# Performance work log

Measured on AMD Instinct MI355X. Metric: run time of the kernel, lower is better.

The kernel has to match this reference:

```python
import jax, jax.numpy as jnp
import numpy as np

# ---------------- config (from ObjectDetector source) ----------------
B = 2; IMG = 224; STRIDE = 32; FH = IMG // STRIDE          # 7x7 feature map
C_FEAT = 1024
SIZES = (32., 64., 128., 256., 512.); RATIOS = (0.5, 1.0, 2.0)
A = len(SIZES) * len(RATIOS)                                # 15 anchors/loc
NA = FH * FH * A                                            # 735 anchors/img
PRE_NMS = min(1000, NA); POST_NMS = min(1000, NA)           # testing config
RPN_NMS_T = 0.7; RPN_MIN_SIZE = 1e-3
NUM_CLASSES = 37
ROI_OUT = 7; ROI_SR = 2; ROI_SCALE = 1.0 / STRIDE
REP = 1024
SCORE_T = 0.05; DET_NMS_T = 0.5; DETS_PER_IMG = 100
CAND_K = 2048            # candidate cap before final batched NMS
MIN_SIZE_DET = 1e-2
BBOX_CLIP = float(np.log(1000.0 / 16.0))


def make_anchors():
    scales = np.array(SIZES, np.float32); ratios = np.array(RATIOS, np.float32)
    h_r = np.sqrt(ratios); w_r = 1.0 / h_r
    ws = (w_r[:, None] * scales[None, :]).reshape(-1)
    hs = (h_r[:, None] * scales[None, :]).reshape(-1)
    base = np.round(np.stack([-ws, -hs, ws, hs], 1) / 2.0)   # [A,4]
    sy, sx = np.meshgrid(np.arange(FH) * STRIDE, np.arange(FH) * STRIDE, indexing='ij')
    shifts = np.stack([sx.reshape(-1), sy.reshape(-1), sx.reshape(-1), sy.reshape(-1)], 1).astype(np.float32)
    return jnp.asarray((shifts[:, None, :] + base[None, :, :]).reshape(-1, 4))  # [NA,4] (H,W,A)


def conv(x, w, b, stride=1, pad=0):
    y = jax.lax.conv_general_dilated(x, w, (stride, stride), [(pad, pad)] * 2,
                                     dimension_numbers=('NCHW', 'OIHW', 'NCHW'))
    return y + b[None, :, None, None]


def decode_boxes(deltas, boxes, weights):
    wx, wy, ww, wh = weights
    w = boxes[..., 2] - boxes[..., 0]; h = boxes[..., 3] - boxes[..., 1]
    cx = boxes[..., 0] + 0.5 * w; cy = boxes[..., 1] + 0.5 * h
    dx = deltas[..., 0] / wx; dy = deltas[..., 1] / wy
    dw = jnp.minimum(deltas[..., 2] / ww, BBOX_CLIP)
    dh = jnp.minimum(deltas[..., 3] / wh, BBOX_CLIP)
    pcx = dx * w + cx; pcy = dy * h + cy
    pw = jnp.exp(dw) * w; ph = jnp.exp(dh) * h
    return jnp.stack([pcx - 0.5 * pw, pcy - 0.5 * ph, pcx + 0.5 * pw, pcy + 0.5 * ph], -1)


def clip_boxes(b):
    x = jnp.clip(b[..., 0::2], 0.0, float(IMG)); y = jnp.clip(b[..., 1::2], 0.0, float(IMG))
    return jnp.stack([x[..., 0], y[..., 0], x[..., 1], y[..., 1]], -1)


def box_iou(a, b):
    area_a = (a[:, 2] - a[:, 0]) * (a[:, 3] - a[:, 1])
    area_b = (b[:, 2] - b[:, 0]) * (b[:, 3] - b[:, 1])
    lt = jnp.maximum(a[:, None, :2], b[None, :, :2])
    rb = jnp.minimum(a[:, None, 2:], b[None, :, 2:])
    wh = jnp.clip(rb - lt, 0.0, None)
    inter = wh[..., 0] * wh[..., 1]
    return inter / jnp.maximum(area_a[:, None] + area_b[None, :] - inter, 1e-9)


def nms_keep(boxes, scores, thresh):
    """Greedy NMS; returns keep mask in original order (fixed shapes)."""
    n = boxes.shape[0]
    order = jnp.argsort(-scores)
    iou = box_iou(*(jax.lax.stop_gradient(boxes[order]),) * 2)
    idx = jnp.arange(n)
    def body(i, keep):
        sup = (iou[i] > thresh) & (idx > i) & keep[i]
        return keep & ~sup
    keep_sorted = jax.lax.fori_loop(0, n, body, jnp.ones(n, bool))
    return jnp.zeros(n, bool).at[order].set(keep_sorted)


def rpn_filter_one(obj_logits, deltas, anchors):
    # obj_logits [NA], deltas [NA,4] (detached, as in torchvision RPN)
    top_v, top_i = jax.lax.top_k(obj_logits, PRE_NMS)
    boxes = clip_boxes(decode_boxes(deltas[top_i], anchors[top_i], (1., 1., 1., 1.)))
    prob = jax.nn.sigmoid(top_v)
    ws = boxes[:, 2] - boxes[:, 0]; hs = boxes[:, 3] - boxes[:, 1]
    prob = jnp.where((ws >= RPN_MIN_SIZE) & (hs >= RPN_MIN_SIZE), prob, -1.0)
    prob = jnp.where(nms_keep(boxes, prob, RPN_NMS_T), prob, -1.0)
    sv, si = jax.lax.top_k(prob, POST_NMS)
    return boxes[si], sv > 0.0


def bilinear(f_hwc, ys, xs):
    # torchvision roi_align bilinear sampling; f_hwc [H,W,C], ys/xs [R,O]
    H, W, _ = f_hwc.shape
    vy = (ys >= -1.0) & (ys <= H); vx = (xs >= -1.0) & (xs <= W)
    y = jnp.clip(ys, 0.0, None); x = jnp.clip(xs, 0.0, None)
    y0 = jnp.minimum(jnp.floor(y).astype(jnp.int32), H - 1)
    x0 = jnp.minimum(jnp.floor(x).astype(jnp.int32), W - 1)
    y1 = jnp.minimum(y0 + 1, H - 1); x1 = jnp.minimum(x0 + 1, W - 1)
    y = jnp.where(y0 == H - 1, y0.astype(y.dtype), y)
    x = jnp.where(x0 == W - 1, x0.astype(x.dtype), x)
    ly = y - y0; lx = x - x0; hy = 1.0 - ly; hx = 1.0 - lx
    g = lambda yi, xi: f_hwc[yi[:, :, None], xi[:, None, :]]   # [R,O,O,C]
    val = ((hy[:, :, None] * hx[:, None, :])[..., None] * g(y0, x0)
         + (hy[:, :, None] * lx[:, None, :])[..., None] * g(y0, x1)
         + (ly[:, :, None] * hx[:, None, :])[..., None] * g(y1, x0)
         + (ly[:, :, None] * lx[:, None, :])[..., None] * g(y1, x1))
    return val * (vy[:, :, None] & vx[:, None, :])[..., None]


def roi_align_one(feat_chw, rois):
    # feat [C,H,W], rois [R,4] -> [R,C,7,7]; output_size=7, sampling_ratio=2, scale=1/32
    f = jnp.transpose(feat_chw, (1, 2, 0))
    x1 = rois[:, 0] * ROI_SCALE; y1 = rois[:, 1] * ROI_SCALE
    rw = jnp.maximum(rois[:, 2] * ROI_SCALE - x1, 1.0)
    rh = jnp.maximum(rois[:, 3] * ROI_SCALE - y1, 1.0)
    bw = rw / ROI_OUT; bh = rh / ROI_OUT
    grid = jnp.arange(ROI_OUT, dtype=jnp.float32)
    acc = 0.0
    for iy in range(ROI_SR):
        ys = y1[:, None] + (grid[None, :] + (iy + 0.5) / ROI_SR) * bh[:, None]
        for ix in range(ROI_SR):
            xs = x1[:, None] + (grid[None, :] + (ix + 0.5) / ROI_SR) * bw[:, None]
            acc = acc + bilinear(f, ys, xs)
    return jnp.transpose(acc / (ROI_SR * ROI_SR), (0, 3, 1, 2))


def postprocess_one(logits, box_deltas, proposals, roi_valid):
    R = logits.shape[0]
    scores = jax.nn.softmax(logits, -1)
    boxes = clip_boxes(decode_boxes(box_deltas.reshape(R, NUM_CLASSES, 4),
                                    proposals[:, None, :], (10., 10., 5., 5.)))
    boxes = boxes[:, 1:, :].reshape(-1, 4)       # drop background class
    scores = jnp.where(roi_valid[:, None], scores[:, 1:], 0.0).reshape(-1)
    labels = jnp.broadcast_to(jnp.arange(1, NUM_CLASSES)[None, :], (R, NUM_CLASSES - 1)).reshape(-1)
    ws = boxes[:, 2] - boxes[:, 0]; hs = boxes[:, 3] - boxes[:, 1]
    ok = (ws >= MIN_SIZE_DET) & (hs >= MIN_SIZE_DET) & (scores > SCORE_T)
    cs, ci = jax.lax.top_k(jnp.where(ok, scores, -1.0), CAND_K)
    cb = boxes[ci]; cl = labels[ci]
    off = cl.astype(cb.dtype) * (IMG + 1.0)      # batched (per-class) NMS trick
    keep = nms_keep(cb + off[:, None], cs, DET_NMS_T)
    tv, ti = jax.lax.top_k(jnp.where(keep, cs, -1.0), DETS_PER_IMG)
    valid = tv > 0.0
    out_boxes = jnp.where(valid[:, None], cb[ti], 0.0)
    out_scores = jnp.where(valid, tv, 0.0)
    out_labels = jnp.where(valid, cl[ti], 0).astype(out_boxes.dtype)
    return jnp.concatenate([out_boxes, out_scores[:, None], out_labels[:, None]], -1)  # [100,6]


def forward(images, params, anchors):
    (bb_w, bb_b, rpn_w, rpn_b, cls_w, cls_b, reg_w, reg_b,
     fc1_w, fc1_b, fc2_w, fc2_b, clsp_w, clsp_b, boxp_w, boxp_b) = params
    Bn = images.shape[0]
    feats = jax.nn.relu(conv(images, bb_w, bb_b, stride=STRIDE))        # [B,1024,7,7]
    t = jax.nn.relu(conv(feats, rpn_w, rpn_b, stride=1, pad=1))
    obj = jnp.transpose(conv(t, cls_w, cls_b), (0, 2, 3, 1)).reshape(Bn, -1)            # [B,NA]
    reg = jnp.transpose(conv(t, reg_w, reg_b).reshape(Bn, A, 4, FH, FH),
                        (0, 3, 4, 1, 2)).reshape(Bn, -1, 4)                              # [B,NA,4]
    obj_d = jax.lax.stop_gradient(obj); reg_d = jax.lax.stop_gradient(reg)  # RPN detaches
    proposals, roi_valid = jax.vmap(lambda o, d: rpn_filter_one(o, d, anchors))(obj_d, reg_d)
    pooled = jax.vmap(roi_align_one)(feats, proposals)                  # [B,R,1024,7,7]
    x = pooled.reshape(Bn * POST_NMS, -1)
    x = jax.nn.relu(x @ fc1_w.T + fc1_b)
    x = jax.nn.relu(x @ fc2_w.T + fc2_b)
    logits = (x @ clsp_w.T + clsp_b).reshape(Bn, POST_NMS, NUM_CLASSES)
    bdelt = (x @ boxp_w.T + boxp_b).reshape(Bn, POST_NMS, NUM_CLASSES * 4)
    return jax.vmap(postprocess_one)(logits, bdelt, proposals, roi_valid)  # [B,100,6]


def setup_inputs() -> dict:
    key = jax.random.key(0)
    ks = jax.random.split(key, 10)
    w = lambda k, shape, s=0.02: jax.random.normal(k, shape, jnp.float32) * s
    return {
        'images': jax.random.uniform(ks[0], (B, 1, IMG, IMG), jnp.float32),
        'bb_w': w(ks[1], (C_FEAT, 1, STRIDE, STRIDE)), 'bb_b': jnp.zeros((C_FEAT,), jnp.float32),
        'rpn_w': w(ks[2], (C_FEAT, C_FEAT, 3, 3)), 'rpn_b': jnp.zeros((C_FEAT,), jnp.float32),
        'cls_w': w(ks[3], (A, C_FEAT, 1, 1)), 'cls_b': jnp.zeros((A,), jnp.float32),
        'reg_w': w(ks[4], (4 * A, C_FEAT, 1, 1)), 'reg_b': jnp.zeros((4 * A,), jnp.float32),
        'fc1_w': w(ks[5], (REP, C_FEAT * ROI_OUT * ROI_OUT), 0.005), 'fc1_b': jnp.zeros((REP,), jnp.float32),
        'fc2_w': w(ks[6], (REP, REP)), 'fc2_b': jnp.zeros((REP,), jnp.float32),
        'clsp_w': w(ks[7], (NUM_CLASSES, REP)), 'clsp_b': jnp.zeros((NUM_CLASSES,), jnp.float32),
        'boxp_w': w(ks[8], (NUM_CLASSES * 4, REP)), 'boxp_b': jnp.zeros((NUM_CLASSES * 4,), jnp.float32),
    }


def reference(images, bb_w, bb_b, rpn_w, rpn_b, cls_w, cls_b, reg_w, reg_b,
              fc1_w, fc1_b, fc2_w, fc2_b, clsp_w, clsp_b, boxp_w, boxp_b):
    anchors = make_anchors()
    params = (bb_w, bb_b, rpn_w, rpn_b, cls_w, cls_b, reg_w, reg_b,
              fc1_w, fc1_b, fc2_w, fc2_b, clsp_w, clsp_b, boxp_w, boxp_b)
    return forward(images, params, anchors)
```

## Files before the change

### kernel.cpp

```cpp
#include <hip/hip_runtime.h>
#include <math.h>

#define NANCH 735
#define NCAND 26460
#define NCANDP 26624
#define BBCLIP 4.135166556742356f
#define KF1 4864
#define KHALF 2432

typedef short bf16x8 __attribute__((ext_vector_type(8)));
typedef float f32x4 __attribute__((ext_vector_type(4)));

__device__ __forceinline__ unsigned short f2b(float f) {
  unsigned int u = __float_as_uint(f);
  unsigned int r = (u >> 16) & 1u;
  u += 0x7fffu + r;
  return (unsigned short)(u >> 16);
}

__device__ __forceinline__ bool before_(float va, int ia, float vb, int ib) {
  return (va > vb) || (va == vb && ia < ib);
}

template<int NTOT, int NTH>
__device__ void bitonic_sort_sh(float* v, int* id) {
  const int t = threadIdx.x;
  for (int k = 2; k <= NTOT; k <<= 1) {
    for (int j = k >> 1; j > 0; j >>= 1) {
      for (int s = t; s < NTOT; s += NTH) {
        int p = s ^ j;
        if (p > s) {
          float v1 = v[s], v2 = v[p];
          int i1 = id[s], i2 = id[p];
          bool up = ((s & k) == 0);
          if (before_(v2, i2, v1, i1) == up) {
            v[s] = v2; id[s] = i2; v[p] = v1; id[p] = i1;
          }
        }
      }
      __syncthreads();
    }
  }
}

template<int NTOT, int NTH>
__device__ void bitonic_merge_sh(float* v, int* id) {
  const int t = threadIdx.x;
  for (int j = NTOT >> 1; j > 0; j >>= 1) {
    for (int s = t; s < NTOT; s += NTH) {
      int p = s ^ j;
      if (p > s) {
        float v1 = v[s], v2 = v[p];
        int i1 = id[s], i2 = id[p];
        if (before_(v2, i2, v1, i1)) {
          v[s] = v2; id[s] = i2; v[p] = v1; id[p] = i1;
        }
      }
    }
    __syncthreads();
  }
}

__global__ void k_anchors(float* __restrict__ anchors) {
  int i = blockIdx.x * 64 + threadIdx.x;
  if (i >= NANCH) return;
  int pos = i / 15, a = i % 15;
  int iy = pos / 7, ix = pos % 7;
  int rr = a / 5, sc = a % 5;
  double ratio = (rr == 0) ? 0.5 : (rr == 1 ? 1.0 : 2.0);
  double scale = (double)(32 << sc);
  double hr = sqrt(ratio), wr = 1.0 / hr;
  double wsz = wr * scale, hsz = hr * scale;
  float bx1 = (float)rint(-wsz * 0.5), by1 = (float)rint(-hsz * 0.5);
  float bx2 = (float)rint(wsz * 0.5),  by2 = (float)rint(hsz * 0.5);
  float sx = (float)(ix * 32), sy = (float)(iy * 32);
  float* o = anchors + (size_t)i * 4;
  o[0] = sx + bx1; o[1] = sy + by1; o[2] = sx + bx2; o[3] = sy + by2;
}

__global__ void k_im2col_bb(const float* __restrict__ images, float* __restrict__ patch) {
  int i = blockIdx.x * 256 + threadIdx.x;
  if (i >= 98 * 1024) return;
  int rowi = i >> 10, k = i & 1023;
  int b = rowi / 49, pos = rowi % 49;
  int oy = pos / 7, ox = pos % 7;
  int ky = k >> 5, kx = k & 31;
  patch[i] = images[((size_t)b * 224 + oy * 32 + ky) * 224 + ox * 32 + kx];
}

__global__ void k_transpose_feats(const float* __restrict__ bbC, float* __restrict__ ft) {
  int i = blockIdx.x * 256 + threadIdx.x;
  if (i >= 2 * 1024 * 49) return;
  int b = i / (1024 * 49);
  int rem = i % (1024 * 49);
  int c = rem / 49, q = rem % 49;
  ft[i] = bbC[((size_t)b * 49 + q) * 1024 + c];
}

__global__ void k_im2col_rpn(const float* __restrict__ ft, float* __restrict__ im2) {
  int i = blockIdx.x * 256 + threadIdx.x;
  if (i >= 98 * 9216) return;
  int rowi = i / 9216, k = i % 9216;
  int b = rowi / 49, pos = rowi % 49;
  int oy = pos / 7, ox = pos % 7;
  int ic = k / 9, kk = k % 9;
  int ky = kk / 3, kx = kk % 3;
  int y = oy + ky - 1, x = ox + kx - 1;
  float v = 0.f;
  if ((unsigned)y < 7u && (unsigned)x < 7u)
    v = ft[((size_t)b * 1024 + ic) * 49 + y * 7 + x];
  im2[i] = v;
}

__global__ __launch_bounds__(256) void k_gemm32(
    const float* __restrict__ A, int lda, int M,
    const float* __restrict__ B, int ldb,
    float* __restrict__ P, int N, int Kchunk)
{
  __shared__ float As[2][16][68];
  __shared__ float Bs[2][16][68];
  const int m0 = blockIdx.x * 64, n0 = blockIdx.y * 64;
  const int t = threadIdx.x;
  const long long k0 = (long long)blockIdx.z * Kchunk;
  float acc[4][4];
#pragma unroll
  for (int i = 0; i < 4; ++i)
#pragma unroll
    for (int j = 0; j < 4; ++j) acc[i][j] = 0.f;
  const int tm = (t >> 4) * 4;
  const int tn = (t & 15) * 4;
  const int sm = t >> 4, sk = t & 15;
  const int gmA = m0 + sm;
  auto ldA = [&](int mo, long long kk) -> float {
    int gm = gmA + mo;
    return (gm < M) ? A[(size_t)gm * lda + k0 + kk + sk] : 0.f;
  };
  auto ldB = [&](int mo, long long kk) -> float {
    return B[(size_t)(n0 + sm + mo) * ldb + k0 + kk + sk];
  };
  const int nt = Kchunk >> 4;
  float a0 = ldA(0, 0), a1 = ldA(16, 0), a2 = ldA(32, 0), a3 = ldA(48, 0);
  float b0 = ldB(0, 0), b1 = ldB(16, 0), b2 = ldB(32, 0), b3 = ldB(48, 0);
  int cur = 0;
  for (int it = 0; it < nt; ++it) {
    As[cur][sk][sm] = a0; As[cur][sk][sm + 16] = a1;
    As[cur][sk][sm + 32] = a2; As[cur][sk][sm + 48] = a3;
    Bs[cur][sk][sm] = b0; Bs[cur][sk][sm + 16] = b1;
    Bs[cur][sk][sm + 32] = b2; Bs[cur][sk][sm + 48] = b3;
    __syncthreads();
    if (it + 1 < nt) {
      long long kk = (long long)(it + 1) * 16;
      a0 = ldA(0, kk); a1 = ldA(16, kk); a2 = ldA(32, kk); a3 = ldA(48, kk);
      b0 = ldB(0, kk); b1 = ldB(16, kk); b2 = ldB(32, kk); b3 = ldB(48, kk);
    }
#pragma unroll
    for (int k = 0; k < 16; ++k) {
      float av[4], bv[4];
#pragma unroll
      for (int i = 0; i < 4; ++i) av[i] = As[cur][k][tm + i];
#pragma unroll
      for (int j = 0; j < 4; ++j) bv[j] = Bs[cur][k][tn + j];
#pragma unroll
      for (int i = 0; i < 4; ++i)
#pragma unroll
        for (int j = 0; j < 4; ++j) acc[i][j] = fmaf(av[i], bv[j], acc[i][j]);
    }
    cur ^= 1;
  }
  float* Pp = P + (size_t)blockIdx.z * M * N;
#pragma unroll
  for (int i = 0; i < 4; ++i) {
    int gm = m0 + tm + i;
    if (gm < M) {
#pragma unroll
      for (int j = 0; j < 4; ++j)
        Pp[(size_t)gm * N + n0 + tn + j] = acc[i][j];
    }
  }
}

__global__ __launch_bounds__(256) void k_gemm_bf16(
    const unsigned short* __restrict__ A, int lda, int M,
    const unsigned short* __restrict__ B, int ldb,
    float* __restrict__ P, int N, int Kchunk,
    const int* __restrict__ nvalid)
{
  __shared__ __attribute__((aligned(16))) unsigned short As[2][128][40];
  __shared__ __attribute__((aligned(16))) unsigned short Bs[2][128][40];
  const int G = gridDim.x * gridDim.y * gridDim.z;
  int lid = blockIdx.x + gridDim.x * (blockIdx.y + gridDim.y * blockIdx.z);
  lid = (lid & 7) * (G >> 3) + (lid >> 3);
  const int bx = lid % gridDim.x;
  const int rest = lid / gridDim.x;
  const int by = rest % gridDim.y, bz = rest / gridDim.y;
  const int m0 = bx * 128, n0 = by * 128;
  if (nvalid) {
    int nv0 = nvalid[0], nv1 = nvalid[1];
    bool ok = (m0 < nv0) || ((m0 + 128 > NANCH) && (m0 < NANCH + nv1));
    if (!ok) return;
  }
  const int t = threadIdx.x;
  const int lane = t & 63, wid = t >> 6;
  const int wm = (wid >> 1) * 64, wn = (wid & 1) * 64;
  const size_t k0 = (size_t)bz * Kchunk;
  f32x4 acc[4][4];
#pragma unroll
  for (int i = 0; i < 4; ++i)
#pragma unroll
    for (int j = 0; j < 4; ++j) acc[i][j] = (f32x4){0.f, 0.f, 0.f, 0.f};
  const int r0 = t >> 2, c0 = (t & 3) * 8;
  const int fr = lane & 15, fk = (lane >> 4) * 8;
  const int gmA0 = m0 + r0, gmA1 = m0 + r0 + 64;
  const bool vA0 = gmA0 < M, vA1 = gmA1 < M;
  const unsigned short* pA0 = A + (size_t)gmA0 * lda + k0 + c0;
  const unsigned short* pA1 = A + (size_t)gmA1 * lda + k0 + c0;
  const unsigned short* pB0 = B + (size_t)(n0 + r0) * ldb + k0 + c0;
  const unsigned short* pB1 = B + (size_t)(n0 + r0 + 64) * ldb + k0 + c0;
  bf16x8 rA0 = {}, rA1 = {}, rB0, rB1;
  if (vA0) rA0 = *(const bf16x8*)pA0;
  if (vA1) rA1 = *(const bf16x8*)pA1;
  rB0 = *(const bf16x8*)pB0;
  rB1 = *(const bf16x8*)pB1;
  const int nt = Kchunk >> 5;
  int cur = 0;
  for (int it = 0; it < nt; ++it) {
    *(bf16x8*)&As[cur][r0][c0] = rA0;
    *(bf16x8*)&As[cur][r0 + 64][c0] = rA1;
    *(bf16x8*)&Bs[cur][r0][c0] = rB0;
    *(bf16x8*)&Bs[cur][r0 + 64][c0] = rB1;
    __syncthreads();
    if (it + 1 < nt) {
      size_t ofs = (size_t)(it + 1) * 32;
      rA0 = vA0 ? *(const bf16x8*)(pA0 + ofs) : (bf16x8){};
      rA1 = vA1 ? *(const bf16x8*)(pA1 + ofs) : (bf16x8){};
      rB0 = *(const bf16x8*)(pB0 + ofs);
      rB1 = *(const bf16x8*)(pB1 + ofs);
    }
    bf16x8 af[4], bg[4];
#pragma unroll
    for (int i = 0; i < 4; ++i) af[i] = *(const bf16x8*)&As[cur][wm + i * 16 + fr][fk];
#pragma unroll
    for (int j = 0; j < 4; ++j) bg[j] = *(const bf16x8*)&Bs[cur][wn + j * 16 + fr][fk];
#pragma unroll
    for (int i = 0; i < 4; ++i)
#pragma unroll
      for (int j = 0; j < 4; ++j)
        acc[i][j] = __builtin_amdgcn_mfma_f32_16x16x32_bf16(af[i], bg[j], acc[i][j], 0, 0, 0);
    cur ^= 1;
  }
  float* Pp = P + (size_t)bz * M * N;
#pragma unroll
  for (int i = 0; i < 4; ++i) {
#pragma unroll
    for (int r = 0; r < 4; ++r) {
      int gm = m0 + wm + i * 16 + (lane >> 4) * 4 + r;
      if (gm < M) {
#pragma unroll
        for (int j = 0; j < 4; ++j)
          Pp[(size_t)gm * N + n0 + wn + j * 16 + (lane & 15)] = acc[i][j][r];
      }
    }
  }
}

__global__ __launch_bounds__(256) void k_gemm_mb(
    const unsigned short* __restrict__ A,
    const unsigned short* __restrict__ W1p,
    float* __restrict__ Mb)
{
  __shared__ __attribute__((aligned(16))) unsigned short As[2][128][40];
  __shared__ __attribute__((aligned(16))) unsigned short Bs[2][128][40];
  const int G = gridDim.x * gridDim.y * gridDim.z;
  int lid = blockIdx.x + gridDim.x * (blockIdx.y + gridDim.y * blockIdx.z);
  lid = (lid & 7) * (G >> 3) + (lid >> 3);
  const int rest = lid;
  const int by = rest % gridDim.y, p = rest / gridDim.y;
  const int n0 = by * 128;
  const int M = 98;
  const unsigned short* B = W1p + (size_t)p * 1048576;
  const int t = threadIdx.x;
  const int lane = t & 63, wid = t >> 6;
  const int wm = (wid >> 1) * 64, wn = (wid & 1) * 64;
  f32x4 acc[4][4];
#pragma unroll
  for (int i = 0; i < 4; ++i)
#pragma unroll
    for (int j = 0; j < 4; ++j) acc[i][j] = (f32x4){0.f, 0.f, 0.f, 0.f};
  const int r0 = t >> 2, c0 = (t & 3) * 8;
  const int fr = lane & 15, fk = (lane >> 4) * 8;
  int gA0 = r0; if (gA0 >= M) gA0 = M - 1;
  int gA1 = r0 + 64; if (gA1 >= M) gA1 = M - 1;
  const unsigned short* pA0 = A + (size_t)gA0 * 1024 + c0;
  const unsigned short* pA1 = A + (size_t)gA1 * 1024 + c0;
  const unsigned short* pB0 = B + (size_t)(n0 + r0) * 1024 + c0;
  const unsigned short* pB1 = B + (size_t)(n0 + r0 + 64) * 1024 + c0;
  bf16x8 rA0 = *(const bf16x8*)pA0;
  bf16x8 rA1 = *(const bf16x8*)pA1;
  bf16x8 rB0 = *(const bf16x8*)pB0;
  bf16x8 rB1 = *(const bf16x8*)pB1;
  const int nt = 1024 >> 5;
  int cur = 0;
  for (int it = 0; it < nt; ++it) {
    *(bf16x8*)&As[cur][r0][c0] = rA0;
    *(bf16x8*)&As[cur][r0 + 64][c0] = rA1;
    *(bf16x8*)&Bs[cur][r0][c0] = rB0;
    *(bf16x8*)&Bs[cur][r0 + 64][c0] = rB1;
    __syncthreads();
    if (it + 1 < nt) {
      size_t ofs = (size_t)(it + 1) * 32;
      rA0 = *(const bf16x8*)(pA0 + ofs);
      rA1 = *(const bf16x8*)(pA1 + ofs);
      rB0 = *(const bf16x8*)(pB0 + ofs);
      rB1 = *(const bf16x8*)(pB1 + ofs);
    }
    bf16x8 af[4], bg[4];
#pragma unroll
    for (int i = 0; i < 4; ++i) af[i] = *(const bf16x8*)&As[cur][wm + i * 16 + fr][fk];
#pragma unroll
    for (int j = 0; j < 4; ++j) bg[j] = *(const bf16x8*)&Bs[cur][wn + j * 16 + fr][fk];
#pragma unroll
    for (int i = 0; i < 4; ++i)
#pragma unroll
      for (int j = 0; j < 4; ++j)
        acc[i][j] = __builtin_amdgcn_mfma_f32_16x16x32_bf16(af[i], bg[j], acc[i][j], 0, 0, 0);
    cur ^= 1;
  }
  float* Pp = Mb + (size_t)p * 98 * 1024;
#pragma unroll
  for (int i = 0; i < 4; ++i) {
#pragma unroll
    for (int r = 0; r < 4; ++r) {
      int gm = wm + i * 16 + (lane >> 4) * 4 + r;
      if (gm < M) {
#pragma unroll
        for (int j = 0; j < 4; ++j)
          Pp[(size_t)gm * 1024 + n0 + wn + j * 16 + (lane & 15)] = acc[i][j][r];
      }
    }
  }
}

__global__ __launch_bounds__(256) void k_mtrans(const float* __restrict__ Mb,
                                                unsigned short* __restrict__ Bmat)
{
  __shared__ float tile[98][129];
  const int p = blockIdx.x, n0 = blockIdx.y * 128;
  const int t = threadIdx.x;
  for (int j = t; j < 98 * 128; j += 256) {
    int q = j >> 7, nl = j & 127;
    tile[q][nl] = Mb[((size_t)p * 98 + q) * 1024 + n0 + nl];
  }
  __syncthreads();
  for (int j = t; j < 128 * 98; j += 256) {
    int nl = j / 98, q2 = j % 98;
    int bb = q2 >= 49 ? 1 : 0;
    int col = bb * KHALF + p * 49 + (q2 - bb * 49);
    Bmat[(size_t)(n0 + nl) * KF1 + col] = f2b(tile[q2][nl]);
  }
  if (p == 0) {
    for (int j = t; j < 128 * 62; j += 256) {
      int nl = j / 62, e = j % 62;
      int bb = e >= 31 ? 1 : 0;
      int col = bb * KHALF + 2401 + (e - bb * 31);
      Bmat[(size_t)(n0 + nl) * KF1 + col] = 0;
    }
  }
}

__global__ __launch_bounds__(256) void k_gbuild(const float* __restrict__ props,
                                                unsigned short* __restrict__ Gmat)
{
#pragma clang fp contract(off)
  int rg = blockIdx.x;
  int b = rg / NANCH;
  __shared__ float g[KF1];
  int t = threadIdx.x;
  for (int j = t; j < KF1; j += 256) g[j] = 0.f;
  __syncthreads();
  if (t < 49) {
    const float* roi = props + (size_t)rg * 4;
    int p = t, oy = p / 7, ox = p % 7;
    float x1 = roi[0] * 0.03125f, y1 = roi[1] * 0.03125f;
    float rw = fmaxf(roi[2] * 0.03125f - x1, 1.f);
    float rh = fmaxf(roi[3] * 0.03125f - y1, 1.f);
    float bw = rw / 7.f, bh = rh / 7.f;
    float* gb = g + b * KHALF + p * 49;
    for (int iy = 0; iy < 2; ++iy) {
      for (int ix = 0; ix < 2; ++ix) {
        float ys = y1 + ((float)oy + ((float)iy + 0.5f) * 0.5f) * bh;
        float xs = x1 + ((float)ox + ((float)ix + 0.5f) * 0.5f) * bw;
        bool vy = (ys >= -1.f) && (ys <= 7.f);
        bool vx = (xs >= -1.f) && (xs <= 7.f);
        float yc = fmaxf(ys, 0.f), xc = fmaxf(xs, 0.f);
        int y0 = min((int)floorf(yc), 6), x0 = min((int)floorf(xc), 6);
        int y1i = min(y0 + 1, 6), x1i = min(x0 + 1, 6);
        if (y0 == 6) yc = 6.f;
        if (x0 == 6) xc = 6.f;
        float ly = yc - (float)y0, lx = xc - (float)x0;
        float hy = 1.f - ly, hx = 1.f - lx;
        float vm = (vy && vx) ? 0.25f : 0.f;
        gb[y0 * 7 + x0]   += hy * hx * vm;
        gb[y0 * 7 + x1i]  += hy * lx * vm;
        gb[y1i * 7 + x0]  += ly * hx * vm;
        gb[y1i * 7 + x1i] += ly * lx * vm;
      }
    }
  }
  __syncthreads();
  unsigned short* Gr = Gmat + (size_t)rg * KF1;
  for (int j = t; j < KF1; j += 256) Gr[j] = f2b(g[j]);
}

__global__ void k_reduce(const float* __restrict__ P, float* __restrict__ dst,
                         unsigned short* __restrict__ dst16,
                         int S, int M, int N, const float* __restrict__ bias, int flags)
{
  size_t i = (size_t)blockIdx.x * 256 + threadIdx.x;
  size_t tot = (size_t)M * N;
  if (i >= tot) return;
  float v = (flags & 1) ? 0.f : dst[i];
  for (int s = 0; s < S; ++s) v += P[(size_t)s * tot + i];
  if (flags & 2) v += bias[i % (size_t)N];
  if (flags & 4) v = fmaxf(v, 0.f);
  dst[i] = v;
  if (flags & 8) dst16[i] = f2b(v);
}

__global__ void k_f2b(const float* __restrict__ s, unsigned short* __restrict__ d, int n) {
  int i = (blockIdx.x * 256 + threadIdx.x) * 4;
  if (i >= n) return;
  float4 v = *(const float4*)(s + i);
  ushort4 o;
  o.x = f2b(v.x); o.y = f2b(v.y); o.z = f2b(v.z); o.w = f2b(v.w);
  *(ushort4*)(d + i) = o;
}

__global__ __launch_bounds__(256) void k_w1perm2(const float* __restrict__ w,
                                                 unsigned short* __restrict__ o)
{
  __shared__ unsigned short tile[128 * 50];
  const int n = blockIdx.x, ct = blockIdx.y;
  const float* src = w + (size_t)n * 50176 + (size_t)ct * 128 * 49;
  const int t = threadIdx.x;
  for (int i = t; i < 6272; i += 256) {
    int cl = i / 49, p = i % 49;
    tile[cl * 50 + p] = f2b(src[i]);
  }
  __syncthreads();
  for (int j = t; j < 6272; j += 256) {
    int p = j >> 7, cl = j & 127;
    o[((size_t)p * 1024 + n) * 1024 + (size_t)ct * 128 + cl] = tile[cl * 50 + p];
  }
}

__global__ __launch_bounds__(256) void k_rpn_head(
    const float* __restrict__ tmn, const float* __restrict__ cls_w,
    const float* __restrict__ cls_b, const float* __restrict__ reg_w,
    const float* __restrict__ reg_b, float* __restrict__ obj, float* __restrict__ reg)
{
  int blk = blockIdx.x;
  __shared__ float col[1024];
  const float* row = tmn + (size_t)blk * 1024;
  for (int i = threadIdx.x; i < 1024; i += 256) col[i] = row[i];
  __syncthreads();
  int b = blk / 49, pos = blk % 49;
  for (int o = threadIdx.x; o < 75; o += 256) {
    const float* w = (o < 15) ? (cls_w + (size_t)o * 1024) : (reg_w + (size_t)(o - 15) * 1024);
    float s = 0.f;
    for (int k = 0; k < 1024; ++k) s = fmaf(col[k], w[k], s);
    if (o < 15) {
      obj[(size_t)b * NANCH + pos * 15 + o] = s + cls_b[o];
    } else {
      int c = o - 15, a = c >> 2, d = c & 3;
      reg[((size_t)b * NANCH + pos * 15 + a) * 4 + d] = s + reg_b[c];
    }
  }
}

__global__ __launch_bounds__(1024) void k_rpn_prep(
    const float* __restrict__ obj, const float* __restrict__ reg,
    const float* __restrict__ anchors,
    float* __restrict__ bxp, float* __restrict__ pnms)
{
#pragma clang fp contract(off)
  const int b = blockIdx.x, t = threadIdx.x;
  __shared__ float sval[1024];
  __shared__ float vo1[1024];
  __shared__ int o1a[1024];
  __shared__ int wtv[16];
  __shared__ int wti[16];
  sval[t] = (t < NANCH) ? obj[(size_t)b * NANCH + t] : -INFINITY;
  __syncthreads();
  {
    float v = sval[t];
    int rank = 0;
    for (int j = 0; j < NANCH; ++j) {
      float u = sval[j];
      rank += (u > v) || (u == v && j < t);
    }
    if (t < NANCH) { vo1[rank] = v; o1a[rank] = t; }
  }
  __syncthreads();
  float x1 = 0.f, y1 = 0.f, x2 = 0.f, y2 = 0.f, prob = -1.f;
  bool flag = false;
  if (t < NANCH) {
    int ai = o1a[t];
    const float* d = reg + ((size_t)b * NANCH + ai) * 4;
    const float* an = anchors + (size_t)ai * 4;
    float aw = an[2] - an[0], ah = an[3] - an[1];
    float acx = an[0] + 0.5f * aw, acy = an[1] + 0.5f * ah;
    float dw = fminf(d[2], BBCLIP), dh = fminf(d[3], BBCLIP);
    float pcx = d[0] * aw + acx, pcy = d[1] * ah + acy;
    float pw = expf(dw) * aw, ph = expf(dh) * ah;
    x1 = pcx - 0.5f * pw; y1 = pcy - 0.5f * ph;
    x2 = pcx + 0.5f * pw; y2 = pcy + 0.5f * ph;
    x1 = fminf(fmaxf(x1, 0.f), 224.f);
    y1 = fminf(fmaxf(y1, 0.f), 224.f);
    x2 = fminf(fmaxf(x2, 0.f), 224.f);
    y2 = fminf(fmaxf(y2, 0.f), 224.f);
    flag = (x2 - x1 >= 1e-3f) && (y2 - y1 >= 1e-3f);
    prob = 1.f / (1.f + expf(-vo1[t]));
  }
  bool iflag = (t < NANCH) && !flag;
  unsigned long long balv = __ballot(flag);
  unsigned long long bali = __ballot(iflag);
  int lane = t & 63, w = t >> 6;
  if (lane == 0) { wtv[w] = __popcll(balv); wti[w] = __popcll(bali); }
  __syncthreads();
  int nval = 0, basev = 0, basei = 0;
  for (int k = 0; k < 16; ++k) {
    int cv = wtv[k], ci = wti[k];
    nval += cv;
    if (k < w) { basev += cv; basei += ci; }
  }
  if (t < NANCH) {
    unsigned long long lm = (1ull << lane) - 1;
    int pos = flag ? (basev + __popcll(balv & lm))
                   : (nval + basei + __popcll(bali & lm));
    float* o = bxp + ((size_t)b * NANCH + pos) * 4;
    o[0] = x1; o[1] = y1; o[2] = x2; o[3] = y2;
    pnms[(size_t)b * NANCH + pos] = flag ? prob : -1.f;
  }
}

__global__ __launch_bounds__(256) void k_rpn_mask(
    const float* __restrict__ bxp, unsigned long long* __restrict__ rmask)
{
#pragma clang fp contract(off)
  int blk = blockIdx.x;
  int b = blk / 35;
  int row = (blk % 35) * 21 + (int)(threadIdx.x / 12);
  int w = threadIdx.x % 12;
  if (threadIdx.x >= 252 || row >= NANCH) return;
  const float* a = bxp + ((size_t)b * NANCH + row) * 4;
  float a0 = a[0], a1 = a[1], a2 = a[2], a3 = a[3];
  float aarea = (a2 - a0) * (a3 - a1);
  int l0 = w * 64;
  int l1 = (l0 + 64 < NANCH) ? l0 + 64 : NANCH;
  int ls = (l0 > row + 1) ? l0 : row + 1;
  unsigned long long bits = 0ull;
  for (int l = ls; l < l1; ++l) {
    const float* q = bxp + ((size_t)b * NANCH + l) * 4;
    float b0 = q[0], b1 = q[1], b2 = q[2], b3 = q[3];
    float barea = (b2 - b0) * (b3 - b1);
    float ix1 = fmaxf(a0, b0), iy1 = fmaxf(a1, b1);
    float ix2 = fminf(a2, b2), iy2 = fminf(a3, b3);
    float iw = fmaxf(ix2 - ix1, 0.f), ih = fmaxf(iy2 - iy1, 0.f);
    float inter = iw * ih;
    float iou = inter / fmaxf(aarea + barea - inter, 1e-9f);
    if (iou > 0.7f) bits |= 1ull << (l & 63);
  }
  rmask[((size_t)b * NANCH + row) * 12 + w] = bits;
}

__global__ __launch_bounds__(1024) void k_rpn_fin(
    const float* __restrict__ bxp, const float* __restrict__ pnms,
    const unsigned long long* __restrict__ rmask,
    float* __restrict__ props, int* __restrict__ meta)
{
  const int b = blockIdx.x, t = threadIdx.x;
  __shared__ unsigned long long smask[NANCH * 12];
  __shared__ float sp[1024];
  __shared__ unsigned long long keepw[12];
  __shared__ int wtot[16];
  for (int i = t; i < NANCH * 12; i += 1024)
    smask[i] = rmask[(size_t)b * NANCH * 12 + i];
  sp[t] = (t < NANCH) ? pnms[(size_t)b * NANCH + t] : -1.f;
  __syncthreads();
  if (t < 64) {
    unsigned long long kl = (t < 12) ? ~0ull : 0ull;
    for (int i = 0; i < NANCH; ++i) {
      unsigned long long kw = __shfl(kl, i >> 6);
      unsigned long long m = (t < 12) ? smask[i * 12 + t] : 0ull;
      bool on = (kw >> (i & 63)) & 1ull;
      kl &= on ? ~m : ~0ull;
    }
    if (t < 12) keepw[t] = kl;
  }
  __syncthreads();
  bool flag = false;
  if (t < NANCH) {
    bool kp = (keepw[t >> 6] >> (t & 63)) & 1ull;
    flag = kp && (sp[t] > 0.f);
  }
  unsigned long long bal = __ballot(flag);
  int lane = t & 63, w = t >> 6;
  if (lane == 0) wtot[w] = __popcll(bal);
  __syncthreads();
  int base = 0, tot = 0;
  for (int k = 0; k < 16; ++k) { int c = wtot[k]; if (k < w) base += c; tot += c; }
  if (flag) {
    int pos = base + __popcll(bal & ((1ull << lane) - 1));
    const float* src = bxp + ((size_t)b * NANCH + t) * 4;
    float* o = props + ((size_t)b * NANCH + pos) * 4;
    o[0] = src[0]; o[1] = src[1]; o[2] = src[2]; o[3] = src[3];
  }
  if (t == 0) meta[b] = tot;
}

__global__ __launch_bounds__(256) void k_heads(
    const float* __restrict__ h2, const float* __restrict__ cw,
    const float* __restrict__ cb, const float* __restrict__ bw_,
    const float* __restrict__ bb_, const int* __restrict__ meta,
    float* __restrict__ logits, float* __restrict__ bdelt)
{
  int rg = blockIdx.x;
  int b = rg / NANCH, r = rg % NANCH;
  if (r >= meta[b]) return;
  __shared__ float row[1024];
  for (int i = threadIdx.x; i < 1024; i += 256) row[i] = h2[(size_t)rg * 1024 + i];
  __syncthreads();
  for (int o = threadIdx.x; o < 185; o += 256) {
    const float* w = (o < 37) ? (cw + (size_t)o * 1024) : (bw_ + (size_t)(o - 37) * 1024);
    float s = 0.f;
    for (int k = 0; k < 1024; ++k) s = fmaf(row[k], w[k], s);
    if (o < 37) logits[(size_t)rg * 37 + o] = s + cb[o];
    else bdelt[(size_t)rg * 148 + (o - 37)] = s + bb_[o - 37];
  }
}

__global__ void k_cand(const float* __restrict__ logits, const float* __restrict__ bdelt,
                       const float* __restrict__ props, const int* __restrict__ meta,
                       float* __restrict__ cscore, float* __restrict__ cbox)
{
#pragma clang fp contract(off)
  int rg = blockIdx.x * blockDim.x + threadIdx.x;
  if (rg >= 2 * NANCH) return;
  int b = rg / NANCH, r = rg % NANCH;
  float* cs = cscore + (size_t)b * NCANDP;
  float* cb = cbox + (size_t)b * NCANDP * 4;
  int base = r * 36;
  if (r >= meta[b]) {
    for (int j = 0; j < 36; ++j) {
      cs[base + j] = -1.f;
      float* q = cb + (size_t)(base + j) * 4;
      q[0] = 0.f; q[1] = 0.f; q[2] = 0.f; q[3] = 0.f;
    }
    return;
  }
  const float* lg = logits + (size_t)rg * 37;
  float mx = lg[0];
// ... 86 lines not shown
      bitonic_merge_sh<2048, 1024>(Lv, Li);
    }
  }
  for (int s = t; s < 2048; s += 1024) {
    sel_score[b * 2048 + s] = Lv[s];
    sel_cidx[b * 2048 + s] = Li[s];
  }
  if (t == 0) meta[2 + b] = 2048;
}

__global__ void k_detmask(const int* __restrict__ sel_cidx,
                          const float* __restrict__ cbox,
                          const int* __restrict__ meta,
                          unsigned long long* __restrict__ dmask)
{
#pragma clang fp contract(off)
  int blk = blockIdx.x;
  int b = blk >> 8, row0 = (blk & 255) * 8;
  int npos = meta[2 + b];
  if (row0 >= npos) return;
  int t = threadIdx.x;
  int i = row0 + (t >> 5), w = t & 31;
  if (i >= npos) return;
  int ci = sel_cidx[b * 2048 + i];
  const float* bp = cbox + ((size_t)b * NCANDP + ci) * 4;
  float off = (float)(ci % 36 + 1) * 225.f;
  float a0 = bp[0] + off, a1 = bp[1] + off, a2 = bp[2] + off, a3 = bp[3] + off;
  float aarea = (a2 - a0) * (a3 - a1);
  unsigned long long bits = 0ull;
  int l0 = w * 64;
  int l1 = (l0 + 64 < npos) ? l0 + 64 : npos;
  int ls = (l0 > i + 1) ? l0 : i + 1;
  for (int l = ls; l < l1; ++l) {
    int cl = sel_cidx[b * 2048 + l];
    const float* q = cbox + ((size_t)b * NCANDP + cl) * 4;
    float o2 = (float)(cl % 36 + 1) * 225.f;
    float b0 = q[0] + o2, b1 = q[1] + o2, b2 = q[2] + o2, b3 = q[3] + o2;
    float barea = (b2 - b0) * (b3 - b1);
    float ix1 = fmaxf(a0, b0), iy1 = fmaxf(a1, b1);
    float ix2 = fminf(a2, b2), iy2 = fminf(a3, b3);
    float iw = fmaxf(ix2 - ix1, 0.f), ih = fmaxf(iy2 - iy1, 0.f);
    float inter = iw * ih;
    float iou = inter / fmaxf(aarea + barea - inter, 1e-9f);
    if (iou > 0.5f) bits |= 1ull << (l & 63);
  }
  dmask[((size_t)b * 2048 + i) * 32 + w] = bits;
}

__global__ __launch_bounds__(1024) void k_final(
    const float* __restrict__ sel_score, const int* __restrict__ sel_cidx,
    const float* __restrict__ cbox, const unsigned long long* __restrict__ dmask,
    const int* __restrict__ meta, float* __restrict__ out)
{
  const int b = blockIdx.x, t = threadIdx.x;
  __shared__ unsigned long long keepw[32];
  __shared__ float sv[2048];
  __shared__ float kv[2048]; __shared__ int ks[2048];
  __shared__ int wtot[32];
  int npos = meta[2 + b];
  for (int h = 0; h < 2; ++h) {
    int s = h * 1024 + t;
    sv[s] = sel_score[b * 2048 + s];
  }
  __syncthreads();
  if (t < 64) {
    unsigned long long kl = (t < 32) ? ~0ull : 0ull;
    for (int i = 0; i < npos; ++i) {
      unsigned long long kw = __shfl(kl, i >> 6);
      unsigned long long m = (t < 32) ? dmask[((size_t)b * 2048 + i) * 32 + t] : 0ull;
      bool on = (kw >> (i & 63)) & 1ull;
      kl &= on ? ~m : ~0ull;
    }
    if (t < 32) keepw[t] = kl;
  }
  __syncthreads();
  const int lane = t & 63, w = t >> 6;
  int s0 = t;
  bool f0 = ((keepw[s0 >> 6] >> (s0 & 63)) & 1ull) && (sv[s0] > 0.f);
  unsigned long long bal0 = __ballot(f0);
  if (lane == 0) wtot[w] = __popcll(bal0);
  int s1 = 1024 + t;
  bool f1 = ((keepw[s1 >> 6] >> (s1 & 63)) & 1ull) && (sv[s1] > 0.f);
  unsigned long long bal1 = __ballot(f1);
  if (lane == 0) wtot[16 + w] = __popcll(bal1);
  __syncthreads();
  int nk = 0, base0 = 0, base1 = 0;
  for (int k = 0; k < 32; ++k) {
    int c = wtot[k];
    if (k < w) base0 += c;
    if (k < 16 + w) base1 += c;
    nk += c;
  }
  int p0 = -1, p1 = -1;
  if (f0) { p0 = base0 + __popcll(bal0 & ((1ull << lane) - 1)); kv[p0] = sv[s0]; ks[p0] = s0; }
  if (f1) { p1 = base1 + __popcll(bal1 & ((1ull << lane) - 1)); kv[p1] = sv[s1]; ks[p1] = s1; }
  __syncthreads();
  if (f0) {
    float v = sv[s0]; int rank = 0;
    for (int j = 0; j < nk; ++j) { float u = kv[j]; int ju = ks[j]; rank += (u > v) || (u == v && ju < s0); }
    if (rank < 100) {
      int ci = sel_cidx[b * 2048 + s0];
      const float* bp = cbox + ((size_t)b * NCANDP + ci) * 4;
      float* o = out + ((size_t)b * 100 + rank) * 6;
      o[0] = bp[0]; o[1] = bp[1]; o[2] = bp[2]; o[3] = bp[3];
      o[4] = v; o[5] = (float)(ci % 36 + 1);
    }
  }
  if (f1) {
    float v = sv[s1]; int rank = 0;
    for (int j = 0; j < nk; ++j) { float u = kv[j]; int ju = ks[j]; rank += (u > v) || (u == v && ju < s1); }
    if (rank < 100) {
      int ci = sel_cidx[b * 2048 + s1];
      const float* bp = cbox + ((size_t)b * NCANDP + ci) * 4;
      float* o = out + ((size_t)b * 100 + rank) * 6;
      o[0] = bp[0]; o[1] = bp[1]; o[2] = bp[2]; o[3] = bp[3];
      o[4] = v; o[5] = (float)(ci % 36 + 1);
    }
  }
  if (t < 100 && t >= nk) {
    float* o = out + ((size_t)b * 100 + t) * 6;
    o[0] = 0.f; o[1] = 0.f; o[2] = 0.f; o[3] = 0.f; o[4] = 0.f; o[5] = 0.f;
  }
}

extern "C" void kernel_launch(void* const* d_in, const int* in_sizes, int n_in,
                              void* d_out, int out_size, void* d_ws, size_t ws_size,
                              hipStream_t stream)
{
  (void)in_sizes; (void)n_in; (void)out_size; (void)ws_size;
  const float* images = (const float*)d_in[0];
  const float* bb_w   = (const float*)d_in[1];
  const float* bb_b   = (const float*)d_in[2];
  const float* rpn_w  = (const float*)d_in[3];
  const float* rpn_b  = (const float*)d_in[4];
  const float* cls_w  = (const float*)d_in[5];
  const float* cls_b  = (const float*)d_in[6];
  const float* reg_w  = (const float*)d_in[7];
  const float* reg_b  = (const float*)d_in[8];
  const float* fc1_w  = (const float*)d_in[9];
  const float* fc1_b  = (const float*)d_in[10];
  const float* fc2_w  = (const float*)d_in[11];
  const float* fc2_b  = (const float*)d_in[12];
  const float* clsp_w = (const float*)d_in[13];
  const float* clsp_b = (const float*)d_in[14];
  const float* boxp_w = (const float*)d_in[15];
  const float* boxp_b = (const float*)d_in[16];
  float* out = (float*)d_out;
  char* ws = (char*)d_ws;

  size_t off = 0;
  auto alloc = [&](size_t bytes) -> size_t {
    size_t o = off; off = (off + bytes + 255) & ~(size_t)255; return o;
  };
  size_t o_anch  = alloc(735ull * 4 * 4);
  size_t o_patch = alloc(98ull * 1024 * 4);
  size_t o_bbC   = alloc(98ull * 1024 * 4);
  size_t o_bbh   = alloc(98ull * 1024 * 2);
  size_t o_ft    = alloc(2ull * 1024 * 49 * 4);
  size_t o_t     = alloc(98ull * 1024 * 4);
  size_t o_im2   = alloc(98ull * 9216 * 4);
  size_t o_obj   = alloc(1470ull * 4);
  size_t o_reg   = alloc(1470ull * 16);
  size_t o_props = alloc(1470ull * 16);
  size_t o_bxp   = alloc(1470ull * 16);
  size_t o_pnms  = alloc(1470ull * 4);
  size_t o_rm    = alloc(1470ull * 12 * 8);
  size_t o_meta  = alloc(256);
  size_t o_y1    = alloc(1470ull * 1024 * 4);
  size_t o_y2    = alloc(1470ull * 1024 * 4);
  size_t o_log   = alloc(1470ull * 37 * 4);
  size_t o_bd    = alloc(1470ull * 148 * 4);
  size_t o_cs    = alloc(2ull * NCANDP * 4);
  size_t o_cb    = alloc(2ull * NCANDP * 16);
  size_t o_ss    = alloc(2ull * 2048 * 4);
  size_t o_sc    = alloc(2ull * 2048 * 4);
  size_t o_dm    = alloc(2ull * 2048 * 32 * 8);
  size_t o_w1p   = alloc(51380224ull * 2);
  size_t o_mbuf  = alloc(49ull * 98 * 1024 * 4);
  size_t o_bmat  = alloc(1024ull * KF1 * 2);
  size_t o_gmat  = alloc(1470ull * KF1 * 2);
  size_t o_w2b   = alloc(1048576ull * 2);
  size_t o_y1b   = alloc(1470ull * 1024 * 2);
  size_t o_P     = alloc(32ull * 98 * 1024 * 4 > 4ull * 1470 * 1024 * 4
                         ? 32ull * 98 * 1024 * 4 : 4ull * 1470 * 1024 * 4);

  float* anch  = (float*)(ws + o_anch);
  float* patch = (float*)(ws + o_patch);
  float* bbC   = (float*)(ws + o_bbC);
  unsigned short* bbh = (unsigned short*)(ws + o_bbh);
  float* ft    = (float*)(ws + o_ft);
  float* tb    = (float*)(ws + o_t);
  float* im2   = (float*)(ws + o_im2);
  float* objb  = (float*)(ws + o_obj);
  float* regb  = (float*)(ws + o_reg);
  float* props = (float*)(ws + o_props);
  float* bxp   = (float*)(ws + o_bxp);
  float* pnms  = (float*)(ws + o_pnms);
  unsigned long long* rmb = (unsigned long long*)(ws + o_rm);
  int*   meta  = (int*)(ws + o_meta);
  float* y1    = (float*)(ws + o_y1);
  float* y2    = (float*)(ws + o_y2);
  float* logb  = (float*)(ws + o_log);
  float* bdb   = (float*)(ws + o_bd);
  float* csb   = (float*)(ws + o_cs);
  float* cbb   = (float*)(ws + o_cb);
  float* ssb   = (float*)(ws + o_ss);
  int*   scb   = (int*)(ws + o_sc);
  unsigned long long* dmb = (unsigned long long*)(ws + o_dm);
  unsigned short* w1p = (unsigned short*)(ws + o_w1p);
  float* mbuf  = (float*)(ws + o_mbuf);
  unsigned short* bmat = (unsigned short*)(ws + o_bmat);
  unsigned short* gmat = (unsigned short*)(ws + o_gmat);
  unsigned short* w2b = (unsigned short*)(ws + o_w2b);
  unsigned short* y1b = (unsigned short*)(ws + o_y1b);
  float* Pb    = (float*)(ws + o_P);

  k_anchors<<<12, 64, 0, stream>>>(anch);
  k_w1perm2<<<dim3(1024, 8), 256, 0, stream>>>(fc1_w, w1p);
  k_f2b<<<1024, 256, 0, stream>>>(fc2_w, w2b, 1048576);
  k_im2col_bb<<<392, 256, 0, stream>>>(images, patch);
  k_gemm32<<<dim3(2, 16, 16), 256, 0, stream>>>(patch, 1024, 98, bb_w, 1024, Pb, 1024, 64);
  k_reduce<<<392, 256, 0, stream>>>(Pb, bbC, bbh, 16, 98, 1024, bb_b, 15);
  k_transpose_feats<<<392, 256, 0, stream>>>(bbC, ft);
  k_gemm_mb<<<dim3(1, 8, 49), 256, 0, stream>>>(bbh, w1p, mbuf);
  k_mtrans<<<dim3(49, 8), 256, 0, stream>>>(mbuf, bmat);
  k_im2col_rpn<<<3528, 256, 0, stream>>>(ft, im2);
  k_gemm32<<<dim3(2, 16, 32), 256, 0, stream>>>(im2, 9216, 98, rpn_w, 9216, Pb, 1024, 288);
  k_reduce<<<392, 256, 0, stream>>>(Pb, tb, nullptr, 32, 98, 1024, rpn_b, 7);
  k_rpn_head<<<98, 256, 0, stream>>>(tb, cls_w, cls_b, reg_w, reg_b, objb, regb);
  k_rpn_prep<<<2, 1024, 0, stream>>>(objb, regb, anch, bxp, pnms);
  k_rpn_mask<<<70, 256, 0, stream>>>(bxp, rmb);
  k_rpn_fin<<<2, 1024, 0, stream>>>(bxp, pnms, rmb, props, meta);
  k_gbuild<<<1470, 256, 0, stream>>>(props, gmat);
  k_gemm_bf16<<<dim3(12, 8, 4), 256, 0, stream>>>(gmat, KF1, 1470, bmat, KF1, Pb, 1024, 1216, meta);
  k_reduce<<<5880, 256, 0, stream>>>(Pb, y1, y1b, 4, 1470, 1024, fc1_b, 15);
  k_gemm_bf16<<<dim3(12, 8, 2), 256, 0, stream>>>(y1b, 1024, 1470, w2b, 1024, Pb, 1024, 512, meta);
  k_reduce<<<5880, 256, 0, stream>>>(Pb, y2, nullptr, 2, 1470, 1024, fc2_b, 7);
  k_heads<<<1470, 256, 0, stream>>>(y2, clsp_w, clsp_b, boxp_w, boxp_b, meta, logb, bdb);
  k_cand<<<6, 256, 0, stream>>>(logb, bdb, props, meta, csb, cbb);
  k_top2048<<<2, 1024, 0, stream>>>(csb, ssb, scb, meta);
  k_detmask<<<512, 256, 0, stream>>>(scb, cbb, meta, dmb);
  k_final<<<2, 1024, 0, stream>>>(ssb, scb, cbb, dmb, meta, out);
}
```

Baseline: 523.0 us.

## Move backbone and RPN conv GEMMs to bf16 MFMA and drop transposes

Replaces the fp32 SIMT GEMM for the backbone patch conv and the 3x3 RPN conv with the existing bf16 MFMA GEMM, converting both weight tensors to bf16 on every call. The im2col buffers become bf16 and the RPN im2col reads the bf16 backbone features directly, which removes the feature transpose kernel. Anchors are now computed inline in the RPN prep kernel, so the anchor kernel and its buffer are gone. In exchange, each call pays for converting about 10M rpn weights, and conv precision drops to bf16, which could shift proposal scores and therefore NMS results.

```diff
diff --git a/kernel.cpp b/kernel.cpp
--- a/kernel.cpp
+++ b/kernel.cpp
@@ -16,6 +16,20 @@
   unsigned int r = (u >> 16) & 1u;
   u += 0x7fffu + r;
   return (unsigned short)(u >> 16);
+}
+
+__device__ __forceinline__ void anchor_of(int i, float* o) {
+  int pos = i / 15, a = i % 15;
+  int iy = pos / 7, ix = pos % 7;
+  int rr = a / 5, sc = a % 5;
+  double ratio = (rr == 0) ? 0.5 : (rr == 1 ? 1.0 : 2.0);
+  double scale = (double)(32 << sc);
+  double hr = sqrt(ratio), wr = 1.0 / hr;
+  double wsz = wr * scale, hsz = hr * scale;
+  float bx1 = (float)rint(-wsz * 0.5), by1 = (float)rint(-hsz * 0.5);
+  float bx2 = (float)rint(wsz * 0.5),  by2 = (float)rint(hsz * 0.5);
+  float sx = (float)(ix * 32), sy = (float)(iy * 32);
+  o[0] = sx + bx1; o[1] = sy + by1; o[2] = sx + bx2; o[3] = sy + by2;
 }
 
 __device__ __forceinline__ bool before_(float va, int ia, float vb, int ib) {
@@ -61,43 +75,18 @@
   }
 }
 
-__global__ void k_anchors(float* __restrict__ anchors) {
-  int i = blockIdx.x * 64 + threadIdx.x;
-  if (i >= NANCH) return;
-  int pos = i / 15, a = i % 15;
-  int iy = pos / 7, ix = pos % 7;
-  int rr = a / 5, sc = a % 5;
-  double ratio = (rr == 0) ? 0.5 : (rr == 1 ? 1.0 : 2.0);
-  double scale = (double)(32 << sc);
-  double hr = sqrt(ratio), wr = 1.0 / hr;
-  double wsz = wr * scale, hsz = hr * scale;
-  float bx1 = (float)rint(-wsz * 0.5), by1 = (float)rint(-hsz * 0.5);
-  float bx2 = (float)rint(wsz * 0.5),  by2 = (float)rint(hsz * 0.5);
-  float sx = (float)(ix * 32), sy = (float)(iy * 32);
-  float* o = anchors + (size_t)i * 4;
-  o[0] = sx + bx1; o[1] = sy + by1; o[2] = sx + bx2; o[3] = sy + by2;
-}
-
-__global__ void k_im2col_bb(const float* __restrict__ images, float* __restrict__ patch) {
+__global__ void k_im2col_bb(const float* __restrict__ images, unsigned short* __restrict__ patch) {
   int i = blockIdx.x * 256 + threadIdx.x;
   if (i >= 98 * 1024) return;
   int rowi = i >> 10, k = i & 1023;
   int b = rowi / 49, pos = rowi % 49;
   int oy = pos / 7, ox = pos % 7;
   int ky = k >> 5, kx = k & 31;
-  patch[i] = images[((size_t)b * 224 + oy * 32 + ky) * 224 + ox * 32 + kx];
-}
-
-__global__ void k_transpose_feats(const float* __restrict__ bbC, float* __restrict__ ft) {
-  int i = blockIdx.x * 256 + threadIdx.x;
-  if (i >= 2 * 1024 * 49) return;
-  int b = i / (1024 * 49);
-  int rem = i % (1024 * 49);
-  int c = rem / 49, q = rem % 49;
-  ft[i] = bbC[((size_t)b * 49 + q) * 1024 + c];
-}
-
-__global__ void k_im2col_rpn(const float* __restrict__ ft, float* __restrict__ im2) {
+  patch[i] = f2b(images[((size_t)b * 224 + oy * 32 + ky) * 224 + ox * 32 + kx]);
+}
+
+__global__ void k_im2col_rpn(const unsigned short* __restrict__ bbh,
+                             unsigned short* __restrict__ im2) {
   int i = blockIdx.x * 256 + threadIdx.x;
   if (i >= 98 * 9216) return;
   int rowi = i / 9216, k = i % 9216;
@@ -106,77 +95,10 @@
   int ic = k / 9, kk = k % 9;
   int ky = kk / 3, kx = kk % 3;
   int y = oy + ky - 1, x = ox + kx - 1;
-  float v = 0.f;
+  unsigned short v = 0;
   if ((unsigned)y < 7u && (unsigned)x < 7u)
-    v = ft[((size_t)b * 1024 + ic) * 49 + y * 7 + x];
+    v = bbh[((size_t)(b * 49 + y * 7 + x)) * 1024 + ic];
   im2[i] = v;
-}
-
-__global__ __launch_bounds__(256) void k_gemm32(
-    const float* __restrict__ A, int lda, int M,
-    const float* __restrict__ B, int ldb,
-    float* __restrict__ P, int N, int Kchunk)
-{
-  __shared__ float As[2][16][68];
-  __shared__ float Bs[2][16][68];
-  const int m0 = blockIdx.x * 64, n0 = blockIdx.y * 64;
-  const int t = threadIdx.x;
-  const long long k0 = (long long)blockIdx.z * Kchunk;
-  float acc[4][4];
-#pragma unroll
-  for (int i = 0; i < 4; ++i)
-#pragma unroll
-    for (int j = 0; j < 4; ++j) acc[i][j] = 0.f;
-  const int tm = (t >> 4) * 4;
-  const int tn = (t & 15) * 4;
-  const int sm = t >> 4, sk = t & 15;
-  const int gmA = m0 + sm;
-  auto ldA = [&](int mo, long long kk) -> float {
-    int gm = gmA + mo;
-    return (gm < M) ? A[(size_t)gm * lda + k0 + kk + sk] : 0.f;
-  };
-  auto ldB = [&](int mo, long long kk) -> float {
-    return B[(size_t)(n0 + sm + mo) * ldb + k0 + kk + sk];
-  };
-  const int nt = Kchunk >> 4;
-  float a0 = ldA(0, 0), a1 = ldA(16, 0), a2 = ldA(32, 0), a3 = ldA(48, 0);
-  float b0 = ldB(0, 0), b1 = ldB(16, 0), b2 = ldB(32, 0), b3 = ldB(48, 0);
-  int cur = 0;
-  for (int it = 0; it < nt; ++it) {
-    As[cur][sk][sm] = a0; As[cur][sk][sm + 16] = a1;
-    As[cur][sk][sm + 32] = a2; As[cur][sk][sm + 48] = a3;
-    Bs[cur][sk][sm] = b0; Bs[cur][sk][sm + 16] = b1;
-    Bs[cur][sk][sm + 32] = b2; Bs[cur][sk][sm + 48] = b3;
-    __syncthreads();
-    if (it + 1 < nt) {
-      long long kk = (long long)(it + 1) * 16;
-      a0 = ldA(0, kk); a1 = ldA(16, kk); a2 = ldA(32, kk); a3 = ldA(48, kk);
-      b0 = ldB(0, kk); b1 = ldB(16, kk); b2 = ldB(32, kk); b3 = ldB(48, kk);
-    }
-#pragma unroll
-    for (int k = 0; k < 16; ++k) {
-      float av[4], bv[4];
-#pragma unroll
-      for (int i = 0; i < 4; ++i) av[i] = As[cur][k][tm + i];
-#pragma unroll
-      for (int j = 0; j < 4; ++j) bv[j] = Bs[cur][k][tn + j];
-#pragma unroll
-      for (int i = 0; i < 4; ++i)
-#pragma unroll
-        for (int j = 0; j < 4; ++j) acc[i][j] = fmaf(av[i], bv[j], acc[i][j]);
-    }
-    cur ^= 1;
-  }
-  float* Pp = P + (size_t)blockIdx.z * M * N;
-#pragma unroll
-  for (int i = 0; i < 4; ++i) {
-    int gm = m0 + tm + i;
-    if (gm < M) {
-#pragma unroll
-      for (int j = 0; j < 4; ++j)
-        Pp[(size_t)gm * N + n0 + tn + j] = acc[i][j];
-    }
-  }
 }
 
 __global__ __launch_bounds__(256) void k_gemm_bf16(
@@ -479,7 +401,6 @@
 
 __global__ __launch_bounds__(1024) void k_rpn_prep(
     const float* __restrict__ obj, const float* __restrict__ reg,
-    const float* __restrict__ anchors,
     float* __restrict__ bxp, float* __restrict__ pnms)
 {
 #pragma clang fp contract(off)
@@ -506,7 +427,8 @@
   if (t < NANCH) {
     int ai = o1a[t];
     const float* d = reg + ((size_t)b * NANCH + ai) * 4;
-    const float* an = anchors + (size_t)ai * 4;
+    float an[4];
+    anchor_of(ai, an);
     float aw = an[2] - an[0], ah = an[3] - an[1];
     float acx = an[0] + 0.5f * aw, acy = an[1] + 0.5f * ah;
     float dw = fminf(d[2], BBCLIP), dh = fminf(d[3], BBCLIP);
@@ -899,13 +821,11 @@
   auto alloc = [&](size_t bytes) -> size_t {
     size_t o = off; off = (off + bytes + 255) & ~(size_t)255; return o;
   };
-  size_t o_anch  = alloc(735ull * 4 * 4);
-  size_t o_patch = alloc(98ull * 1024 * 4);
+  size_t o_patch = alloc(98ull * 1024 * 2);
   size_t o_bbC   = alloc(98ull * 1024 * 4);
   size_t o_bbh   = alloc(98ull * 1024 * 2);
-  size_t o_ft    = alloc(2ull * 1024 * 49 * 4);
   size_t o_t     = alloc(98ull * 1024 * 4);
-  size_t o_im2   = alloc(98ull * 9216 * 4);
+  size_t o_im2   = alloc(98ull * 9216 * 2);
   size_t o_obj   = alloc(1470ull * 4);
   size_t o_reg   = alloc(1470ull * 16);
   size_t o_props = alloc(1470ull * 16);
@@ -922,6 +842,8 @@
   size_t o_ss    = alloc(2ull * 2048 * 4);
   size_t o_sc    = alloc(2ull * 2048 * 4);
   size_t o_dm    = alloc(2ull * 2048 * 32 * 8);
+  size_t o_w0b   = alloc(1048576ull * 2);
+  size_t o_w3b   = alloc(9437184ull * 2);
   size_t o_w1p   = alloc(51380224ull * 2);
   size_t o_mbuf  = alloc(49ull * 98 * 1024 * 4);
   size_t o_bmat  = alloc(1024ull * KF1 * 2);
@@ -931,13 +853,11 @@
   size_t o_P     = alloc(32ull * 98 * 1024 * 4 > 4ull * 1470 * 1024 * 4
                          ? 32ull * 98 * 1024 * 4 : 4ull * 1470 * 1024 * 4);
 
-  float* anch  = (float*)(ws + o_anch);
-  float* patch = (float*)(ws + o_patch);
+  unsigned short* patchb = (unsigned short*)(ws + o_patch);
   float* bbC   = (float*)(ws + o_bbC);
   unsigned short* bbh = (unsigned short*)(ws + o_bbh);
-  float* ft    = (float*)(ws + o_ft);
   float* tb    = (float*)(ws + o_t);
-  float* im2   = (float*)(ws + o_im2);
+  unsigned short* im2b = (unsigned short*)(ws + o_im2);
   float* objb  = (float*)(ws + o_obj);
   float* regb  = (float*)(ws + o_reg);
   float* props = (float*)(ws + o_props);
@@ -954,6 +874,8 @@
   float* ssb   = (float*)(ws + o_ss);
   int*   scb   = (int*)(ws + o_sc);
   unsigned long long* dmb = (unsigned long long*)(ws + o_dm);
+  unsigned short* w0b = (unsigned short*)(ws + o_w0b);
+  unsigned short* w3b = (unsigned short*)(ws + o_w3b);
   unsigned short* w1p = (unsigned short*)(ws + o_w1p);
   float* mbuf  = (float*)(ws + o_mbuf);
   unsigned short* bmat = (unsigned short*)(ws + o_bmat);
@@ -962,20 +884,20 @@
   unsigned short* y1b = (unsigned short*)(ws + o_y1b);
   float* Pb    = (float*)(ws + o_P);
 
-  k_anchors<<<12, 64, 0, stream>>>(anch);
   k_w1perm2<<<dim3(1024, 8), 256, 0, stream>>>(fc1_w, w1p);
   k_f2b<<<1024, 256, 0, stream>>>(fc2_w, w2b, 1048576);
-  k_im2col_bb<<<392, 256, 0, stream>>>(images, patch);
-  k_gemm32<<<dim3(2, 16, 16), 256, 0, stream>>>(patch, 1024, 98, bb_w, 1024, Pb, 1024, 64);
-  k_reduce<<<392, 256, 0, stream>>>(Pb, bbC, bbh, 16, 98, 1024, bb_b, 15);
-  k_transpose_feats<<<392, 256, 0, stream>>>(bbC, ft);
+  k_f2b<<<1024, 256, 0, stream>>>(bb_w, w0b, 1048576);
+  k_f2b<<<9216, 256, 0, stream>>>(rpn_w, w3b, 9437184);
+  k_im2col_bb<<<392, 256, 0, stream>>>(images, patchb);
+  k_gemm_bf16<<<dim3(1, 8, 8), 256, 0, stream>>>(patchb, 1024, 98, w0b, 1024, Pb, 1024, 128, nullptr);
+  k_reduce<<<392, 256, 0, stream>>>(Pb, bbC, bbh, 8, 98, 1024, bb_b, 15);
   k_gemm_mb<<<dim3(1, 8, 49), 256, 0, stream>>>(bbh, w1p, mbuf);
   k_mtrans<<<dim3(49, 8), 256, 0, stream>>>(mbuf, bmat);
-  k_im2col_rpn<<<3528, 256, 0, stream>>>(ft, im2);
-  k_gemm32<<<dim3(2, 16, 32), 256, 0, stream>>>(im2, 9216, 98, rpn_w, 9216, Pb, 1024, 288);
+  k_im2col_rpn<<<3528, 256, 0, stream>>>(bbh, im2b);
+  k_gemm_bf16<<<dim3(1, 8, 32), 256, 0, stream>>>(im2b, 9216, 98, w3b, 9216, Pb, 1024, 288, nullptr);
   k_reduce<<<392, 256, 0, stream>>>(Pb, tb, nullptr, 32, 98, 1024, rpn_b, 7);
   k_rpn_head<<<98, 256, 0, stream>>>(tb, cls_w, cls_b, reg_w, reg_b, objb, regb);
-  k_rpn_prep<<<2, 1024, 0, stream>>>(objb, regb, anch, bxp, pnms);
+  k_rpn_prep<<<2, 1024, 0, stream>>>(objb, regb, bxp, pnms);
   k_rpn_mask<<<70, 256, 0, stream>>>(bxp, rmb);
   k_rpn_fin<<<2, 1024, 0, stream>>>(bxp, pnms, rmb, props, meta);
   k_gbuild<<<1470, 256, 0, stream>>>(props, gmat);
```

After: 503.4 us. 1.04x faster.
